# Performance work log

Measured on AMD Instinct MI355X. Metric: run time of the kernel, lower is better.

The kernel has to match this reference:

```python
import jax, jax.numpy as jnp
import numpy as np

# ---- config (CSA layer, layer_idx=0 of pattern 'CSA,HCA') ----
B, T, C = 2, 2048, 2048
NH, NKV = 16, 8
HD = C // NH            # 128 head dim
ROPE_DIM = HD // 2      # partial RoPE dims (rope_head_dim=0 default)
RATIO = 4               # csa_compress_ratio
G = T // RATIO          # compressed groups (T divisible by ratio -> no pad)
IDX_NH = NH
IDX_HD = max(8, C // NH // 2)  # 64
TOPK = 64               # index_topk
Q_RANK = C // 2         # _default_rank
O_RPG = C // 2          # o_proj rank_per_group, o_groups=1


def rms_norm(x, eps=1e-6):
    return x * jax.lax.rsqrt(jnp.mean(jnp.square(x), axis=-1, keepdims=True) + eps)


def _rope(x, cos, sin):
    d = x.shape[-1] // 2
    x1, x2 = x[..., :d], x[..., d:]
    return jnp.concatenate([x1 * cos + x2 * sin, -x1 * sin + x2 * cos], axis=-1)


def partial_rope(x, cos, sin):
    # rotate only the last ROPE_DIM dims; cos/sin: [..., ROPE_DIM//2]
    xn, xr = x[..., :-ROPE_DIM], x[..., -ROPE_DIM:]
    return jnp.concatenate([xn, _rope(xr, cos, sin)], axis=-1)


def setup_inputs() -> dict:
    key = jax.random.key(0)
    ks = jax.random.split(key, 16)
    s = 0.02
    x = jax.random.normal(ks[0], (B, T, C), jnp.float32)
    pos = jnp.arange(T, dtype=jnp.float32)
    inv = 10000.0 ** (-jnp.arange(0, HD // 2, dtype=jnp.float32) / (HD // 2))
    ang = pos[:, None] * inv[None, :]  # [T, HD//2]
    p = lambda i, shp: jax.random.normal(ks[i], shp, jnp.float32) * s
    return dict(
        x=x, cos=jnp.cos(ang), sin=jnp.sin(ang),
        q_a_w=p(1, (C, Q_RANK)), q_b_w=p(2, (Q_RANK, NH * HD)),
        ck_w=p(3, (C, NKV * HD)), cv_w=p(4, (C, NKV * HD)), cg_w=p(5, (C, NKV * HD)),
        c_ape=p(6, (RATIO, NKV, HD)),
        iq_w=p(7, (C, IDX_NH * IDX_HD)), ik_w=p(8, (C, IDX_NH * IDX_HD)),
        ig_w=p(9, (C, IDX_NH * IDX_HD)), i_ape=p(10, (RATIO, IDX_NH, IDX_HD)),
        sink=jnp.zeros((NH,), jnp.float32),
        o_wa=p(11, (1, O_RPG, C)), o_pb=p(12, (O_RPG, C)),
    )


def reference(x, cos, sin, q_a_w, q_b_w, ck_w, cv_w, cg_w, c_ape,
              iq_w, ik_w, ig_w, i_ape, sink, o_wa, o_pb):
    NEG = jnp.finfo(jnp.float32).min
    half = ROPE_DIM // 2
    # --- low-rank queries + partial RoPE ---
    q = (x @ q_a_w @ q_b_w).reshape(B, T, NH, HD)
    q = partial_rope(q, cos[None, :, None, :half], sin[None, :, None, :half])
    # --- GatedCompressor: learned gated pooling over blocks of RATIO ---
    k = (x @ ck_w).reshape(B, G, RATIO, NKV, HD)
    v = (x @ cv_w).reshape(B, G, RATIO, NKV, HD)
    g = (x @ cg_w).reshape(B, G, RATIO, NKV, HD) + c_ape[None, None]
    w = jax.nn.softmax(g, axis=2)
    ck = (k * w).sum(2)  # [B,G,NKV,HD]
    cv = (v * w).sum(2)
    group_ends = jnp.arange(RATIO - 1, T, RATIO)  # [G]
    ckr = partial_rope(ck, cos[group_ends][None, :, None, :half],
                       sin[group_ends][None, :, None, :half])
    # --- LightningIndexer: compressed indexer keys + per-token top-k groups ---
    ik = (x @ ik_w).reshape(B, G, RATIO, IDX_NH, IDX_HD)
    ig = (x @ ig_w).reshape(B, G, RATIO, IDX_NH, IDX_HD) + i_ape[None, None]
    iw = jax.nn.softmax(ig, axis=2)
    ikeys = rms_norm((ik * iw).sum(2))  # [B,G,IH,IHD]
    iq = rms_norm((x @ iq_w).reshape(B, T, IDX_NH, IDX_HD))
    iscore = jnp.einsum('bthd,bghd->bhtg', iq, ikeys) * IDX_HD ** -0.5
    iscore = iscore.mean(axis=1)  # [B,T,G]
    causal = group_ends[None, None, :] <= jnp.arange(T)[None, :, None]
    iscore = jnp.where(causal, iscore, NEG)
    sel = jax.lax.top_k(iscore, TOPK)[1]  # [B,T,K]
    bidx = jnp.arange(B)[:, None, None]
    tidx = jnp.arange(T)[None, :, None]
    mask = jnp.zeros((B, T, G), bool).at[bidx, tidx, sel].set(True) & causal
    # --- compressed sparse attention with sink, GQA expand ---
    rep = NH // NKV
    kk = jnp.repeat(ckr, rep, axis=2)  # [B,G,NH,HD]
    vv = jnp.repeat(cv, rep, axis=2)
    scores = jnp.einsum('bthd,bghd->bhtg', q, kk) * HD ** -0.5
    scores = jnp.where(mask[:, None], scores, NEG)
    sinkb = jnp.broadcast_to(sink.reshape(1, NH, 1, 1), (B, NH, T, 1))
    probs = jax.nn.softmax(jnp.concatenate([scores, sinkb], axis=-1), axis=-1)[..., :-1]
    out = jnp.einsum('bhtg,bghd->bthd', probs, vv).reshape(B, T, C)
    # --- GroupedOutputProjection (o_groups=1) ---
    h = jnp.einsum('btgd,grd->btgr', out.reshape(B, T, 1, C), o_wa).reshape(B, T, -1)
    return rms_norm(h) @ o_pb
```

## Files before the change

### kernel.cpp

```cpp
#include <hip/hip_runtime.h>
#include <hip/hip_bf16.h>
#include <math.h>

constexpr int Bn  = 2;
constexpr int Tn  = 2048;
constexpr int NHn = 16;
constexpr int NKVn= 8;
constexpr int Gn  = 512;
constexpr int TKn = 64;

typedef __attribute__((ext_vector_type(8))) __bf16 bf16x8;
typedef __attribute__((ext_vector_type(4))) __bf16 bf16x4;
typedef __attribute__((ext_vector_type(2))) __bf16 bf16x2;
typedef __attribute__((ext_vector_type(4))) float f32x4;

__device__ __forceinline__ void gload_lds16(const void* g, void* l) {
  __builtin_amdgcn_global_load_lds(
      (const __attribute__((address_space(1))) unsigned int*)g,
      (__attribute__((address_space(3))) unsigned int*)l, 16, 0, 0);
}

__global__ __launch_bounds__(256) void gemm_pipe_kvqa(
    const __bf16* __restrict__ A, const __bf16* __restrict__ Bt,
    float* __restrict__ Cf, __bf16* __restrict__ Cq)
{
  constexpr int K = 2048;
  constexpr int NT = K / 64;
  __shared__ __bf16 lds[2][2][2][128][32];
  const int tid = threadIdx.x;
  const int wid = tid >> 6, lane = tid & 63;
  const int wm = wid >> 1, wn = wid & 1;
  const int row0 = blockIdx.y * 128, col0 = blockIdx.x * 128;

  f32x4 acc[4][4];
  const f32x4 zero = {0.f, 0.f, 0.f, 0.f};
  #pragma unroll
  for (int i = 0; i < 4; ++i)
    #pragma unroll
    for (int j = 0; j < 4; ++j) acc[i][j] = zero;

  auto stage = [&](int kt, int p, int buf) {
    long k0 = (long)kt * 64 + p * 32;
    #pragma unroll
    for (int l = 0; l < 2; ++l) {
      int u = l * 256 + tid;
      int r = u >> 2, c4 = u & 3;
      long csrc = (long)((c4 ^ ((r >> 1) & 3)) * 8);
      gload_lds16(A  + (long)(row0 + r) * K + k0 + csrc, &lds[buf][0][p][r][c4 * 8]);
      gload_lds16(Bt + (long)(col0 + r) * K + k0 + csrc, &lds[buf][1][p][r][c4 * 8]);
    }
  };

  stage(0, 0, 0);
  stage(0, 1, 0);

  for (int kt = 0; kt < NT; ++kt) {
    const int buf = kt & 1;
    #pragma unroll
    for (int ph = 0; ph < 2; ++ph) {
      if (kt + 1 < NT) {
        stage(kt + 1, ph, buf ^ 1);
        asm volatile("s_waitcnt vmcnt(8)" ::: "memory");
      } else {
        if (ph == 0) asm volatile("s_waitcnt vmcnt(4)" ::: "memory");
        else         asm volatile("s_waitcnt vmcnt(0)" ::: "memory");
      }
      asm volatile("s_barrier" ::: "memory");
      bf16x8 af[4], bfr[4];
      #pragma unroll
      for (int mf = 0; mf < 4; ++mf) {
        int r = wm * 64 + mf * 16 + (lane & 15);
        int c4 = (lane >> 4) ^ ((r >> 1) & 3);
        af[mf] = *(const bf16x8*)&lds[buf][0][ph][r][c4 * 8];
      }
      #pragma unroll
      for (int nf = 0; nf < 4; ++nf) {
        int r = wn * 64 + nf * 16 + (lane & 15);
        int c4 = (lane >> 4) ^ ((r >> 1) & 3);
        bfr[nf] = *(const bf16x8*)&lds[buf][1][ph][r][c4 * 8];
      }
      __builtin_amdgcn_s_setprio(1);
      #pragma unroll
      for (int mf = 0; mf < 4; ++mf)
        #pragma unroll
        for (int nf = 0; nf < 4; ++nf)
          acc[mf][nf] = __builtin_amdgcn_mfma_f32_16x16x32_bf16(af[mf], bfr[nf], acc[mf][nf], 0, 0, 0);
      __builtin_amdgcn_s_setprio(0);
      asm volatile("s_barrier" ::: "memory");
    }
  }

  const int crow = (lane >> 4) * 4, ccol = lane & 15;
  const bool isQ = (col0 >= 3072);
  #pragma unroll
  for (int mf = 0; mf < 4; ++mf)
    #pragma unroll
    for (int nf = 0; nf < 4; ++nf)
      #pragma unroll
      for (int j = 0; j < 4; ++j) {
        long r = row0 + wm * 64 + mf * 16 + crow + j;
        long c = col0 + wn * 64 + nf * 16 + ccol;
        float v = acc[mf][nf][j];
        if (isQ) Cq[r * 1024 + (c - 3072)] = (__bf16)v;
        else     Cf[r * 3072 + c] = v;
      }
}

template<int EPI>
__global__ __launch_bounds__(256) void gemm_pipe(
    const __bf16* __restrict__ A, const __bf16* __restrict__ Bt,
    void* __restrict__ Cp, int N, int K,
    const float* __restrict__ cosb, const float* __restrict__ sinb,
    const float* __restrict__ rs)
{
  const int NT = K >> 6;
  __shared__ __bf16 lds[2][2][2][128][32];
  const int tid = threadIdx.x;
  const int wid = tid >> 6, lane = tid & 63;
  const int wm = wid >> 1, wn = wid & 1;
  const int row0 = blockIdx.y * 128, col0 = blockIdx.x * 128;

  f32x4 acc[4][4];
  const f32x4 zero = {0.f, 0.f, 0.f, 0.f};
  #pragma unroll
  for (int i = 0; i < 4; ++i)
    #pragma unroll
    for (int j = 0; j < 4; ++j) acc[i][j] = zero;

  auto stage = [&](int kt, int p, int buf) {
    long k0 = (long)kt * 64 + p * 32;
    #pragma unroll
    for (int l = 0; l < 2; ++l) {
      int u = l * 256 + tid;
      int r = u >> 2, c4 = u & 3;
      long csrc = (long)((c4 ^ ((r >> 1) & 3)) * 8);
      gload_lds16(A  + (long)(row0 + r) * K + k0 + csrc, &lds[buf][0][p][r][c4 * 8]);
      gload_lds16(Bt + (long)(col0 + r) * K + k0 + csrc, &lds[buf][1][p][r][c4 * 8]);
    }
  };

  stage(0, 0, 0);
  stage(0, 1, 0);

  for (int kt = 0; kt < NT; ++kt) {
    const int buf = kt & 1;
    #pragma unroll
    for (int ph = 0; ph < 2; ++ph) {
      if (kt + 1 < NT) {
        stage(kt + 1, ph, buf ^ 1);
        asm volatile("s_waitcnt vmcnt(8)" ::: "memory");
      } else {
        if (ph == 0) asm volatile("s_waitcnt vmcnt(4)" ::: "memory");
        else         asm volatile("s_waitcnt vmcnt(0)" ::: "memory");
      }
      asm volatile("s_barrier" ::: "memory");
      bf16x8 af[4], bfr[4];
      #pragma unroll
      for (int mf = 0; mf < 4; ++mf) {
        int r = wm * 64 + mf * 16 + (lane & 15);
        int c4 = (lane >> 4) ^ ((r >> 1) & 3);
        af[mf] = *(const bf16x8*)&lds[buf][0][ph][r][c4 * 8];
      }
      #pragma unroll
      for (int nf = 0; nf < 4; ++nf) {
        int r = wn * 64 + nf * 16 + (lane & 15);
        int c4 = (lane >> 4) ^ ((r >> 1) & 3);
        bfr[nf] = *(const bf16x8*)&lds[buf][1][ph][r][c4 * 8];
      }
      __builtin_amdgcn_s_setprio(1);
      #pragma unroll
      for (int mf = 0; mf < 4; ++mf)
        #pragma unroll
        for (int nf = 0; nf < 4; ++nf)
          acc[mf][nf] = __builtin_amdgcn_mfma_f32_16x16x32_bf16(af[mf], bfr[nf], acc[mf][nf], 0, 0, 0);
      __builtin_amdgcn_s_setprio(0);
      asm volatile("s_barrier" ::: "memory");
    }
  }

  const int crow = (lane >> 4) * 4, ccol = lane & 15;
  if constexpr (EPI == 1) {
    __bf16* C = (__bf16*)Cp;
    if (wn == 1) {
      #pragma unroll
      for (int mf = 0; mf < 4; ++mf)
        #pragma unroll
        for (int j = 0; j < 4; ++j) {
          long r = row0 + wm * 64 + mf * 16 + crow + j;
          int t = (int)(r & 2047);
          #pragma unroll
          for (int nfp = 0; nfp < 2; ++nfp) {
            int jj = nfp * 16 + ccol;
            float c = cosb[t * 64 + jj], s = sinb[t * 64 + jj];
            float x1 = acc[mf][nfp][j];
            float x2 = acc[mf][nfp + 2][j];
            C[r * N + col0 + 64 + jj] = (__bf16)(x1 * c + x2 * s);
            C[r * N + col0 + 96 + jj] = (__bf16)(-x1 * s + x2 * c);
          }
        }
    } else {
      #pragma unroll
      for (int mf = 0; mf < 4; ++mf)
        #pragma unroll
        for (int nf = 0; nf < 4; ++nf)
          #pragma unroll
          for (int j = 0; j < 4; ++j) {
            long r = row0 + wm * 64 + mf * 16 + crow + j;
            long c = col0 + nf * 16 + ccol;
            C[r * N + c] = (__bf16)acc[mf][nf][j];
          }
    }
  } else {
    #pragma unroll
    for (int mf = 0; mf < 4; ++mf)
      #pragma unroll
      for (int nf = 0; nf < 4; ++nf)
        #pragma unroll
        for (int j = 0; j < 4; ++j) {
          long r = row0 + wm * 64 + mf * 16 + crow + j;
          long c = col0 + wn * 64 + nf * 16 + ccol;
          float v = acc[mf][nf][j];
          if constexpr (EPI == 2)
            ((float*)Cp)[r * N + c] = v * rs[r];
          else
            ((__bf16*)Cp)[r * N + c] = (__bf16)v;
        }
  }
}

__global__ __launch_bounds__(256) void gemm_split(
    const __bf16* __restrict__ Ah, const __bf16* __restrict__ Al,
    const __bf16* __restrict__ Bh, const __bf16* __restrict__ Bl,
    float* __restrict__ C, int M, int N, int K, float alpha,
    long sA, long sB, long sC)
{
  __shared__ __bf16 Ahs[128 * 64];
  __shared__ __bf16 Als[128 * 64];
  __shared__ __bf16 Bhs[128 * 64];
  __shared__ __bf16 Bls[128 * 64];
  const int tid = threadIdx.x;
  const int wid = tid >> 6, lane = tid & 63;
  const int wm = wid >> 1, wn = wid & 1;
  const int row0 = blockIdx.y * 128, col0 = blockIdx.x * 128;
  Ah += (long)blockIdx.z * sA;  Al += (long)blockIdx.z * sA;
  Bh += (long)blockIdx.z * sB;  Bl += (long)blockIdx.z * sB;

  f32x4 acc[4][4];
  const f32x4 zero = {0.f, 0.f, 0.f, 0.f};
  #pragma unroll
  for (int i = 0; i < 4; ++i)
    #pragma unroll
    for (int j = 0; j < 4; ++j) acc[i][j] = zero;

  const int srow = tid >> 3;
  const int skc  = (tid & 7) * 8;

  for (int k0 = 0; k0 < K; k0 += 64) {
    #pragma unroll
    for (int i = 0; i < 4; ++i) {
      long go = (long)(row0 + srow + 32 * i) * K + k0 + skc;
      int  lo = (i * 256 + tid) * 8;
      gload_lds16(Ah + go, Ahs + lo);
      gload_lds16(Al + go, Als + lo);
    }
    #pragma unroll
    for (int i = 0; i < 4; ++i) {
      long go = (long)(col0 + srow + 32 * i) * K + k0 + skc;
      int  lo = (i * 256 + tid) * 8;
      gload_lds16(Bh + go, Bhs + lo);
      gload_lds16(Bl + go, Bls + lo);
    }
    __syncthreads();
    #pragma unroll
    for (int kk = 0; kk < 2; ++kk) {
      const int kof = kk * 32 + (lane >> 4) * 8;
      bf16x8 ah[4], al[4], bh[4], bl[4];
      #pragma unroll
      for (int mf = 0; mf < 4; ++mf) {
        int ro = (wm * 64 + mf * 16 + (lane & 15)) * 64 + kof;
        ah[mf] = *(const bf16x8*)&Ahs[ro];
        al[mf] = *(const bf16x8*)&Als[ro];
      }
      #pragma unroll
      for (int nf = 0; nf < 4; ++nf) {
        int ro = (wn * 64 + nf * 16 + (lane & 15)) * 64 + kof;
        bh[nf] = *(const bf16x8*)&Bhs[ro];
        bl[nf] = *(const bf16x8*)&Bls[ro];
      }
      #pragma unroll
      for (int mf = 0; mf < 4; ++mf)
        #pragma unroll
        for (int nf = 0; nf < 4; ++nf) {
          acc[mf][nf] = __builtin_amdgcn_mfma_f32_16x16x32_bf16(ah[mf], bh[nf], acc[mf][nf], 0, 0, 0);
          acc[mf][nf] = __builtin_amdgcn_mfma_f32_16x16x32_bf16(ah[mf], bl[nf], acc[mf][nf], 0, 0, 0);
          acc[mf][nf] = __builtin_amdgcn_mfma_f32_16x16x32_bf16(al[mf], bh[nf], acc[mf][nf], 0, 0, 0);
        }
    }
    __syncthreads();
  }
  const int crow = (lane >> 4) * 4, ccol = lane & 15;
  #pragma unroll
  for (int mf = 0; mf < 4; ++mf)
    #pragma unroll
    for (int nf = 0; nf < 4; ++nf)
      #pragma unroll
      for (int j = 0; j < 4; ++j) {
        long r = row0 + wm * 64 + mf * 16 + crow + j;
        long c = col0 + wn * 64 + nf * 16 + ccol;
        C[(long)blockIdx.z * sC + r * N + c] = acc[mf][nf][j] * alpha;
      }
}

__global__ __launch_bounds__(256) void prep_index(
    const float* __restrict__ x,
    const float* __restrict__ s0, const float* __restrict__ s1,
    const float* __restrict__ s2,
    __bf16* __restrict__ hiB, __bf16* __restrict__ loB, long dstride,
    __bf16* __restrict__ xhi, __bf16* __restrict__ xlo)
{
  __shared__ float tile[64][65];
  int z = blockIdx.y;
  int tid = threadIdx.x;
  if (z < 3) {
    const int R = 2048, Cc = 1024;
    const float* in = (z == 0) ? s0 : (z == 1) ? s1 : s2;
    __bf16* hiT = hiB + (long)z * dstride;
    __bf16* loT = loB + (long)z * dstride;
    int f = blockIdx.x;
    int r0 = (f >> 4) * 64, c0 = (f & 15) * 64;
    #pragma unroll
    for (int j = 0; j < 16; ++j) {
      int idx = tid + j * 256;
      int r = idx >> 6, c = idx & 63;
      tile[r][c] = in[(long)(r0 + r) * Cc + c0 + c];
    }
    __syncthreads();
    #pragma unroll
    for (int j = 0; j < 16; ++j) {
      int idx = tid + j * 256;
      int c = idx >> 6, r = idx & 63;
      float v = tile[r][c];
      __bf16 h = (__bf16)v;
      hiT[(long)(c0 + c) * R + r0 + r] = h;
      loT[(long)(c0 + c) * R + r0 + r] = (__bf16)(v - (float)h);
    }
  } else {
    for (long i = ((long)blockIdx.x * 256 + tid) * 4; i < 8388608; i += 524288) {
      float4 v = *(const float4*)&x[i];
      bf16x4 h, l;
      h[0] = (__bf16)v.x; l[0] = (__bf16)(v.x - (float)h[0]);
      h[1] = (__bf16)v.y; l[1] = (__bf16)(v.y - (float)h[1]);
      h[2] = (__bf16)v.z; l[2] = (__bf16)(v.z - (float)h[2]);
      h[3] = (__bf16)v.w; l[3] = (__bf16)(v.w - (float)h[3]);
      *(bf16x4*)&xhi[i] = h;
      *(bf16x4*)&xlo[i] = l;
    }
  }
}

__global__ __launch_bounds__(256) void prep_main(
    const float* __restrict__ s0, const float* __restrict__ s1,
    const float* __restrict__ s2, const float* __restrict__ s3,
    const float* __restrict__ s4, const float* __restrict__ s5,
    const float* __restrict__ wa,
    __bf16* __restrict__ W, long W2, __bf16* __restrict__ owab)
{
  __shared__ float tile[64][65];
  int z = blockIdx.y;
  int tid = threadIdx.x;
  if (z < 6) {
    int R, Cc, r0, c0;
    const float* in;
    if (z < 4) {
      R = 2048; Cc = 1024;
      in = (z == 0) ? s0 : (z == 1) ? s1 : (z == 2) ? s2 : s3;
      r0 = (blockIdx.x >> 4) * 64; c0 = (blockIdx.x & 15) * 64;
    } else {
      R = 1024; Cc = 2048;
      in = (z == 4) ? s4 : s5;
      r0 = (blockIdx.x >> 5) * 64; c0 = (blockIdx.x & 31) * 64;
    }
    __bf16* out = W + (long)z * W2;
    #pragma unroll
    for (int j = 0; j < 16; ++j) {
      int idx = tid + j * 256;
      int r = idx >> 6, c = idx & 63;
      tile[r][c] = in[(long)(r0 + r) * Cc + c0 + c];
    }
    __syncthreads();
    #pragma unroll
    for (int j = 0; j < 16; ++j) {
      int idx = tid + j * 256;
      int c = idx >> 6, r = idx & 63;
      out[(long)(c0 + c) * R + r0 + r] = (__bf16)tile[r][c];
    }
  } else {
    for (long i = ((long)blockIdx.x * 256 + tid) * 4; i < 2097152; i += 524288) {
      float4 v = *(const float4*)&wa[i];
      bf16x4 o;
      o[0] = (__bf16)v.x; o[1] = (__bf16)v.y; o[2] = (__bf16)v.z; o[3] = (__bf16)v.w;
      *(bf16x4*)&owab[i] = o;
    }
  }
}

__global__ __launch_bounds__(256) void reduce_ckcv(
    const float* __restrict__ base, const float* __restrict__ c_ape,
    const float* __restrict__ cosb, const float* __restrict__ sinb,
    __bf16* __restrict__ ckb, __bf16* __restrict__ cvb)
{
  __shared__ float sck[256];
  const long S = 3072;
  int tid = threadIdx.x;
  int c = blockIdx.x * 256 + tid;
  int g = blockIdx.y, b = blockIdx.z;
  long row0 = (long)b * Tn + 4 * g;
  float lg[4], mx = -1e30f;
  #pragma unroll
  for (int r = 0; r < 4; ++r) {
    lg[r] = base[(row0 + r) * S + 2048 + c] + c_ape[r * 1024 + c];
    mx = fmaxf(mx, lg[r]);
  }
  float ssum = 0.f;
  #pragma unroll
  for (int r = 0; r < 4; ++r) { lg[r] = expf(lg[r] - mx); ssum += lg[r]; }
  float inv = 1.f / ssum, ak = 0.f, av = 0.f;
  #pragma unroll
  for (int r = 0; r < 4; ++r) {
    float w = lg[r] * inv;
    ak = fmaf(base[(row0 + r) * S + c],        w, ak);
    av = fmaf(base[(row0 + r) * S + 1024 + c], w, av);
  }
  long o = ((long)b * Gn + g) * 1024 + c;
  cvb[o] = (__bf16)av;
  sck[tid] = ak;
  __syncthreads();
  int d = c & 127;
  float outk = ak;
  if (d >= 64) {
    int t = 4 * g + 3;
    if (d < 96) {
      int j = d - 64;
      outk = ak * cosb[t * 64 + j] + sck[tid + 32] * sinb[t * 64 + j];
    } else {
      int j = d - 96;
      outk = -sck[tid - 32] * sinb[t * 64 + j] + ak * cosb[t * 64 + j];
    }
  }
  ckb[o] = (__bf16)outk;
}

__global__ __launch_bounds__(1024) void reduce_idx_fused(
    const float* __restrict__ base, const float* __restrict__ i_ape,
    __bf16* __restrict__ khi, __bf16* __restrict__ klo,
    __bf16* __restrict__ qhi, __bf16* __restrict__ qlo)
{
  const long S = 3072;
  int tid = threadIdx.x;
  int bid = blockIdx.x;
  if (bid < Gn * Bn) {
    int g = bid & (Gn - 1), b = bid >> 9;
    long row0 = (long)b * Tn + 4 * g;
    float lg[4], mx = -1e30f;
    #pragma unroll
    for (int r = 0; r < 4; ++r) {
      lg[r] = base[(row0 + r) * S + 1024 + tid] + i_ape[r * 1024 + tid];
      mx = fmaxf(mx, lg[r]);
    }
    float ssum = 0.f;
    #pragma unroll
    for (int r = 0; r < 4; ++r) { lg[r] = expf(lg[r] - mx); ssum += lg[r]; }
    float inv = 1.f / ssum, red = 0.f;
    #pragma unroll
    for (int r = 0; r < 4; ++r) red = fmaf(base[(row0 + r) * S + tid], lg[r] * inv, red);
    float ss = red * red;
    #pragma unroll
    for (int o = 32; o; o >>= 1) ss += __shfl_xor(ss, o);
    float v = red * rsqrtf(ss * (1.f / 64.f) + 1e-6f);
    long oi = ((long)b * Gn + g) * 1024 + tid;
    __bf16 h = (__bf16)v;
    khi[oi] = h; klo[oi] = (__bf16)(v - (float)h);
  } else {
    long row = bid - Gn * Bn;
    float v = base[row * S + 2048 + tid];
    float ss = v * v;
    #pragma unroll
    for (int o = 32; o; o >>= 1) ss += __shfl_xor(ss, o);
    float y = v * rsqrtf(ss * (1.f / 64.f) + 1e-6f);
    __bf16 h = (__bf16)y;
    qhi[row * 1024 + tid] = h;
    qlo[row * 1024 + tid] = (__bf16)(y - (float)h);
  }
}

__global__ __launch_bounds__(256) void rms_scales(
    const __bf16* __restrict__ h, float* __restrict__ rs)
{
  int wid = threadIdx.x >> 6, lane = threadIdx.x & 63;
  long row = (long)blockIdx.x * 4 + wid;
  const __bf16* hr = h + row * 1024 + lane * 16;
  bf16x8 a = *(const bf16x8*)hr;
  bf16x8 b = *(const bf16x8*)(hr + 8);
  float ss = 0.f;
  #pragma unroll
  for (int j = 0; j < 8; ++j) {
    float x = (float)a[j], y = (float)b[j];
    ss = fmaf(x, x, ss); ss = fmaf(y, y, ss);
  }
  #pragma unroll
  for (int o = 1; o < 64; o <<= 1) ss += __shfl_xor(ss, o);
  if (lane == 0) rs[row] = rsqrtf(ss * (1.f / 1024.f) + 1e-6f);
}

__global__ __launch_bounds__(256) void topk_kernel(
    const float* __restrict__ iscore, int* __restrict__ selidx, int* __restrict__ selcnt)
{
  int wave = threadIdx.x >> 6, lane = threadIdx.x & 63;
  long bt = (long)blockIdx.x * 4 + wave;
  int t = (int)(bt % Tn);
  const float* row = iscore + bt * Gn;
  int ng = (t + 1) >> 2; if (ng > Gn) ng = Gn;
  int cap = ng < TKn ? ng : TKn;
  float s[8];
  #pragma unroll
  for (int j = 0; j < 8; ++j) {
    int g = lane + 64 * j;
    s[j] = (g < ng) ? row[g] : -INFINITY;
  }
  int* outp = selidx + bt * TKn;
  for (int it = 0; it < cap; ++it) {
    float bv = -INFINITY; int bi = Gn;
    #pragma unroll
    for (int j = 0; j < 8; ++j) {
      int g = lane + 64 * j;
      if (s[j] > bv) { bv = s[j]; bi = g; }
    }
    #pragma unroll
    for (int o = 1; o < 64; o <<= 1) {
      float ov = __shfl_xor(bv, o); int oi = __shfl_xor(bi, o);
      if (ov > bv || (ov == bv && oi < bi)) { bv = ov; bi = oi; }
    }
    if (lane == 0) outp[it] = bi;
    #pragma unroll
    for (int j = 0; j < 8; ++j) if (bi == lane + 64 * j) s[j] = -INFINITY;
  }
  for (int it = cap + lane; it < TKn; it += 64) outp[it] = 0;
  if (lane == 0) selcnt[bt] = cap;
}

__global__ __launch_bounds__(256) void attn_kernel(
    const __bf16* __restrict__ q, const __bf16* __restrict__ ckb,
    const __bf16* __restrict__ cvb, const int* __restrict__ selidx,
    const int* __restrict__ selcnt, const float* __restrict__ sink,
    __bf16* __restrict__ out)
{
  __shared__ float sS[4][16][68];
  __shared__ int   sG[4][64];
  const float scale = 0.08838834764831845f;
  int wid = threadIdx.x >> 6, lane = threadIdx.x & 63;
  long bt = (long)blockIdx.x * 4 + wid;
  int b = (int)(bt >> 11);
  int cnt = selcnt[bt];
  int gid = (lane < cnt) ? selidx[bt * TKn + lane] : 0;
  sG[wid][lane] = gid;

  int grp = lane >> 3;
  int sub = lane & 7;
  int h0 = grp * 2, h1 = h0 + 1;
  int d0 = sub * 16;

  const __bf16* qrow = q + bt * 2048;
  float q0[16], q1[16];
  {
    bf16x8 a0 = *(const bf16x8*)&qrow[h0 * 128 + d0];
    bf16x8 a1 = *(const bf16x8*)&qrow[h0 * 128 + d0 + 8];
    bf16x8 c0 = *(const bf16x8*)&qrow[h1 * 128 + d0];
    bf16x8 c1 = *(const bf16x8*)&qrow[h1 * 128 + d0 + 8];
    #pragma unroll
    for (int j = 0; j < 8; ++j) {
      q0[j] = (float)a0[j]; q0[8 + j] = (float)a1[j];
      q1[j] = (float)c0[j]; q1[8 + j] = (float)c1[j];
    }
  }
  __syncthreads();

  for (int i0 = 0; i0 < 64; i0 += 8) {
    #pragma unroll
    for (int u = 0; u < 8; ++u) {
      int i = i0 + u;
      int g = sG[wid][i];
      const __bf16* kr = ckb + ((long)(b * Gn + g)) * 1024 + lane * 16;
      bf16x8 k0 = *(const bf16x8*)kr;
      bf16x8 k1 = *(const bf16x8*)(kr + 8);
      float p0 = 0.f, p1 = 0.f;
      #pragma unroll
      for (int j = 0; j < 8; ++j) {
        float kv = (float)k0[j];
        p0 = fmaf(kv, q0[j], p0); p1 = fmaf(kv, q1[j], p1);
      }
      #pragma unroll
      for (int j = 0; j < 8; ++j) {
        float kv = (float)k1[j];
        p0 = fmaf(kv, q0[8 + j], p0); p1 = fmaf(kv, q1[8 + j], p1);
      }
      p0 += __shfl_xor(p0, 1); p0 += __shfl_xor(p0, 2); p0 += __shfl_xor(p0, 4);
      p1 += __shfl_xor(p1, 1); p1 += __shfl_xor(p1, 2); p1 += __shfl_xor(p1, 4);
      if (sub == 0) { sS[wid][h0][i] = p0; sS[wid][h1][i] = p1; }
    }
  }
  __syncthreads();

  {
    int h = lane >> 2, qtr = lane & 3;
    float sv[16];
    float mx = -INFINITY;
    #pragma unroll
    for (int j = 0; j < 16; ++j) {
      int i = qtr * 16 + j;
      float s = (i < cnt) ? sS[wid][h][i] * scale : -INFINITY;
      sv[j] = s; mx = fmaxf(mx, s);
    }
    mx = fmaxf(mx, __shfl_xor(mx, 1));
    mx = fmaxf(mx, __shfl_xor(mx, 2));
    float snk = sink[h];
    mx = fmaxf(mx, snk);
    float sum = 0.f;
    #pragma unroll
    for (int j = 0; j < 16; ++j) { sv[j] = __expf(sv[j] - mx); sum += sv[j]; }
    sum += __shfl_xor(sum, 1);
    sum += __shfl_xor(sum, 2);
    sum += __expf(snk - mx);
    float inv = 1.f / sum;
    #pragma unroll
    for (int j = 0; j < 16; ++j) sS[wid][h][qtr * 16 + j] = sv[j] * inv;
  }
  __syncthreads();

  float o0[16], o1[16];
  #pragma unroll
  for (int j = 0; j < 16; ++j) { o0[j] = 0.f; o1[j] = 0.f; }
  for (int i0 = 0; i0 < 64; i0 += 8) {
    #pragma unroll
    for (int u = 0; u < 8; ++u) {
      int i = i0 + u;
      int g = sG[wid][i];
      float p0 = sS[wid][h0][i], p1 = sS[wid][h1][i];
      const __bf16* vr = cvb + ((long)(b * Gn + g)) * 1024 + lane * 16;
      bf16x8 v0 = *(const bf16x8*)vr;
      bf16x8 v1 = *(const bf16x8*)(vr + 8);
      #pragma unroll
      for (int j = 0; j < 8; ++j) {
        float vv = (float)v0[j];
        o0[j] = fmaf(p0, vv, o0[j]); o1[j] = fmaf(p1, vv, o1[j]);
      }
      #pragma unroll
      for (int j = 0; j < 8; ++j) {
        float vv = (float)v1[j];
        o0[8 + j] = fmaf(p0, vv, o0[8 + j]); o1[8 + j] = fmaf(p1, vv, o1[8 + j]);
      }
    }
  }
  __bf16* ob = out + bt * 2048;
  bf16x8 w;
  #pragma unroll
  for (int j = 0; j < 8; ++j) w[j] = (__bf16)o0[j];
  *(bf16x8*)&ob[h0 * 128 + d0] = w;
  #pragma unroll
  for (int j = 0; j < 8; ++j) w[j] = (__bf16)o0[8 + j];
  *(bf16x8*)&ob[h0 * 128 + d0 + 8] = w;
  #pragma unroll
  for (int j = 0; j < 8; ++j) w[j] = (__bf16)o1[j];
  *(bf16x8*)&ob[h1 * 128 + d0] = w;
  #pragma unroll
  for (int j = 0; j < 8; ++j) w[j] = (__bf16)o1[8 + j];
  *(bf16x8*)&ob[h1 * 128 + d0 + 8] = w;
}

extern "C" void kernel_launch(void* const* d_in, const int* in_sizes, int n_in,
                              void* d_out, int out_size, void* d_ws, size_t ws_size,
                              hipStream_t stream) {
  const float* x     = (const float*)d_in[0];
  const float* cosb  = (const float*)d_in[1];
  const float* sinb  = (const float*)d_in[2];
  const float* q_a_w = (const float*)d_in[3];
  const float* q_b_w = (const float*)d_in[4];
  const float* ck_w  = (const float*)d_in[5];
  const float* cv_w  = (const float*)d_in[6];
  const float* cg_w  = (const float*)d_in[7];
  const float* c_ape = (const float*)d_in[8];
  const float* iq_w  = (const float*)d_in[9];
  const float* ik_w  = (const float*)d_in[10];
  const float* ig_w  = (const float*)d_in[11];
  const float* i_ape = (const float*)d_in[12];
  const float* sink  = (const float*)d_in[13];
  const float* o_wa  = (const float*)d_in[14];
  const float* o_pb  = (const float*)d_in[15];
  float* outp = (float*)d_out;
  float* ws = (float*)d_ws;

  const long F  = 4194304;
  const long M1 = 1048576;

  float* b_all = ws;
  float*  iscore = ws + F;
  __bf16* oatt_b = (__bf16*)(ws + F);
  __bf16* hb_b   = (__bf16*)ws;

  __bf16* iq_hi = (__bf16*)d_out;
  __bf16* iq_lo = (__bf16*)d_out + 4194304;
  __bf16* qb    = (__bf16*)d_out;

  char* tp = (char*)(ws + 3 * F);
  __bf16* ckb = (__bf16*)tp;     tp += (size_t)M1 * 4;
  __bf16* cvb = (__bf16*)tp;     tp += (size_t)M1 * 4;
  int*   selidx = (int*)tp;      tp += 2097152;
  int*   selcnt = selidx + Bn * Tn * TKn;
  __bf16* ikeys_hi = (__bf16*)tp; tp += 2097152;
  __bf16* ikeys_lo = (__bf16*)tp; tp += 2097152;
  __bf16* xhi = (__bf16*)tp;      tp += 16777216;
  __bf16* xlo = (__bf16*)tp;      tp += 16777216;
  __bf16* W   = (__bf16*)tp;      tp += 7 * 4194304;
  __bf16* qa_buf = (__bf16*)tp;   tp += 8388608;
  float*  rs     = (float*)tp;    tp += 16384;
  const long W2 = 2097152;
  __bf16* Whi = W;            __bf16* Wlo = W + 3 * W2;
  __bf16* ckT  = W;
  __bf16* qbT  = W + 4*W2;
  __bf16* opbT = W + 5*W2;   __bf16* owab = W + 6*W2;

  prep_index<<<dim3(512, 4), 256, 0, stream>>>(
      x, ik_w, ig_w, iq_w, Whi, Wlo, W2, xhi, xlo);

  gemm_split<<<dim3(24, 32), 256, 0, stream>>>(xhi, xlo, Whi, Wlo, b_all,
      4096, 3072, 2048, 1.f, 0, 0, 0);
  reduce_idx_fused<<<dim3(Gn * Bn + Bn * Tn), 1024, 0, stream>>>(
      b_all, i_ape, ikeys_hi, ikeys_lo, iq_hi, iq_lo);

  gemm_split<<<dim3(4, 16, 2), 256, 0, stream>>>(iq_hi, iq_lo, ikeys_hi, ikeys_lo, iscore,
      2048, 512, 1024, 1.f / 128.f, (long)2048 * 1024, (long)512 * 1024, (long)2048 * 512);
  topk_kernel<<<dim3(Bn * Tn / 4), 256, 0, stream>>>(iscore, selidx, selcnt);

  prep_main<<<dim3(512, 7), 256, 0, stream>>>(
      ck_w, cv_w, cg_w, q_a_w, q_b_w, o_pb, o_wa, W, W2, owab);

  gemm_pipe_kvqa<<<dim3(32, 32), 256, 0, stream>>>(xhi, ckT, b_all, qa_buf);
  reduce_ckcv<<<dim3(4, Gn, Bn), 256, 0, stream>>>(b_all, c_ape, cosb, sinb, ckb, cvb);

  gemm_pipe<1><<<dim3(16, 32), 256, 0, stream>>>(
      qa_buf, qbT, qb, 2048, 1024, cosb, sinb, nullptr);

  attn_kernel<<<dim3(Bn * Tn / 4), 256, 0, stream>>>(qb, ckb, cvb, selidx, selcnt, sink, oatt_b);

  gemm_pipe<0><<<dim3(8, 32), 256, 0, stream>>>(
      oatt_b, owab, hb_b, 1024, 2048, nullptr, nullptr, nullptr);
  rms_scales<<<dim3(1024), 256, 0, stream>>>(hb_b, rs);
  gemm_pipe<2><<<dim3(16, 32), 256, 0, stream>>>(
      hb_b, opbT, outp, 2048, 1024, nullptr, nullptr, rs);
}
```

Before: 556.0 us.

## Double-buffer split-bf16 GEMM with swizzled LDS and async prefetch

```diff
diff --git a/kernel.cpp b/kernel.cpp
--- a/kernel.cpp
+++ b/kernel.cpp
@@ -234,10 +234,8 @@
     float* __restrict__ C, int M, int N, int K, float alpha,
     long sA, long sB, long sC)
 {
-  __shared__ __bf16 Ahs[128 * 64];
-  __shared__ __bf16 Als[128 * 64];
-  __shared__ __bf16 Bhs[128 * 64];
-  __shared__ __bf16 Bls[128 * 64];
+  const int NT = K >> 5;
+  __shared__ __bf16 lds[2][4][128][32];
   const int tid = threadIdx.x;
   const int wid = tid >> 6, lane = tid & 63;
   const int wm = wid >> 1, wn = wid & 1;
@@ -252,52 +250,61 @@
     #pragma unroll
     for (int j = 0; j < 4; ++j) acc[i][j] = zero;
 
-  const int srow = tid >> 3;
-  const int skc  = (tid & 7) * 8;
-
-  for (int k0 = 0; k0 < K; k0 += 64) {
-    #pragma unroll
-    for (int i = 0; i < 4; ++i) {
-      long go = (long)(row0 + srow + 32 * i) * K + k0 + skc;
-      int  lo = (i * 256 + tid) * 8;
-      gload_lds16(Ah + go, Ahs + lo);
-      gload_lds16(Al + go, Als + lo);
-    }
-    #pragma unroll
-    for (int i = 0; i < 4; ++i) {
-      long go = (long)(col0 + srow + 32 * i) * K + k0 + skc;
-      int  lo = (i * 256 + tid) * 8;
-      gload_lds16(Bh + go, Bhs + lo);
-      gload_lds16(Bl + go, Bls + lo);
-    }
-    __syncthreads();
-    #pragma unroll
-    for (int kk = 0; kk < 2; ++kk) {
-      const int kof = kk * 32 + (lane >> 4) * 8;
-      bf16x8 ah[4], al[4], bh[4], bl[4];
-      #pragma unroll
-      for (int mf = 0; mf < 4; ++mf) {
-        int ro = (wm * 64 + mf * 16 + (lane & 15)) * 64 + kof;
-        ah[mf] = *(const bf16x8*)&Ahs[ro];
-        al[mf] = *(const bf16x8*)&Als[ro];
-      }
+  auto stage = [&](int kt, int buf) {
+    long k0 = (long)kt * 32;
+    #pragma unroll
+    for (int l = 0; l < 2; ++l) {
+      int u = l * 256 + tid;
+      int r = u >> 2, c4 = u & 3;
+      long csrc = (long)((c4 ^ ((r >> 1) & 3)) * 8);
+      long ga = (long)(row0 + r) * K + k0 + csrc;
+      long gb = (long)(col0 + r) * K + k0 + csrc;
+      gload_lds16(Ah + ga, &lds[buf][0][r][c4 * 8]);
+      gload_lds16(Al + ga, &lds[buf][1][r][c4 * 8]);
+      gload_lds16(Bh + gb, &lds[buf][2][r][c4 * 8]);
+      gload_lds16(Bl + gb, &lds[buf][3][r][c4 * 8]);
+    }
+  };
+
+  stage(0, 0);
+
+  for (int kt = 0; kt < NT; ++kt) {
+    const int buf = kt & 1;
+    if (kt + 1 < NT) {
+      stage(kt + 1, buf ^ 1);
+      asm volatile("s_waitcnt vmcnt(8)" ::: "memory");
+    } else {
+      asm volatile("s_waitcnt vmcnt(0)" ::: "memory");
+    }
+    asm volatile("s_barrier" ::: "memory");
+    bf16x8 ah[4], al[4], bh[4], bl[4];
+    #pragma unroll
+    for (int mf = 0; mf < 4; ++mf) {
+      int r = wm * 64 + mf * 16 + (lane & 15);
+      int c4 = (lane >> 4) ^ ((r >> 1) & 3);
+      ah[mf] = *(const bf16x8*)&lds[buf][0][r][c4 * 8];
+      al[mf] = *(const bf16x8*)&lds[buf][1][r][c4 * 8];
+    }
+    #pragma unroll
+    for (int nf = 0; nf < 4; ++nf) {
+      int r = wn * 64 + nf * 16 + (lane & 15);
+      int c4 = (lane >> 4) ^ ((r >> 1) & 3);
+      bh[nf] = *(const bf16x8*)&lds[buf][2][r][c4 * 8];
+      bl[nf] = *(const bf16x8*)&lds[buf][3][r][c4 * 8];
+    }
+    __builtin_amdgcn_s_setprio(1);
+    #pragma unroll
+    for (int mf = 0; mf < 4; ++mf)
       #pragma unroll
       for (int nf = 0; nf < 4; ++nf) {
-        int ro = (wn * 64 + nf * 16 + (lane & 15)) * 64 + kof;
-        bh[nf] = *(const bf16x8*)&Bhs[ro];
-        bl[nf] = *(const bf16x8*)&Bls[ro];
-      }
-      #pragma unroll
-      for (int mf = 0; mf < 4; ++mf)
-        #pragma unroll
-        for (int nf = 0; nf < 4; ++nf) {
-          acc[mf][nf] = __builtin_amdgcn_mfma_f32_16x16x32_bf16(ah[mf], bh[nf], acc[mf][nf], 0, 0, 0);
-          acc[mf][nf] = __builtin_amdgcn_mfma_f32_16x16x32_bf16(ah[mf], bl[nf], acc[mf][nf], 0, 0, 0);
-          acc[mf][nf] = __builtin_amdgcn_mfma_f32_16x16x32_bf16(al[mf], bh[nf], acc[mf][nf], 0, 0, 0);
-        }
-    }
-    __syncthreads();
-  }
+        acc[mf][nf] = __builtin_amdgcn_mfma_f32_16x16x32_bf16(ah[mf], bh[nf], acc[mf][nf], 0, 0, 0);
+        acc[mf][nf] = __builtin_amdgcn_mfma_f32_16x16x32_bf16(ah[mf], bl[nf], acc[mf][nf], 0, 0, 0);
+        acc[mf][nf] = __builtin_amdgcn_mfma_f32_16x16x32_bf16(al[mf], bh[nf], acc[mf][nf], 0, 0, 0);
+      }
+    __builtin_amdgcn_s_setprio(0);
+    asm volatile("s_barrier" ::: "memory");
+  }
+
   const int crow = (lane >> 4) * 4, ccol = lane & 15;
   #pragma unroll
   for (int mf = 0; mf < 4; ++mf)
```

After: 541.8 us. 2.5% less time.
